# Kernel optimization log

Hardware: AMD Instinct MI355X
Metric: run time of the kernel (lower is better)

Reference implementation:

```python
import jax, jax.numpy as jnp
import numpy as np

H, W = 480, 640
NUM_CLASSES = 3
SKIP = 5            # skip_pixels: stride between voting pixels
GRID = 8            # stride of Hough accumulator bins
LABEL_THRESHOLD = 5
INLIER_THRESHOLD = 0.5
VOTING_THRESHOLD = 0.3


def setup_inputs():
    key = jax.random.key(0)
    k1, k2, k3, k4 = jax.random.split(key, 4)
    bottom_label = jax.random.randint(k1, (1, H, W), 0, NUM_CLASSES).astype(jnp.int32)
    bottom_vertex = jax.random.normal(k2, (1, NUM_CLASSES * 3, H, W), jnp.float32)
    bottom_meta_data = jax.random.normal(k3, (1, 10), jnp.float32)
    extents = jax.random.normal(k4, (NUM_CLASSES, 3), jnp.float32)
    return {"bottom_label": bottom_label, "bottom_vertex": bottom_vertex,
            "bottom_meta_data": bottom_meta_data, "extents": extents}


def _hough_voting(bottom_label, bottom_vertex, bottom_meta_data, extents):
    label = bottom_label[0]                                   # [H,W] int
    vert = bottom_vertex[0].reshape(NUM_CLASSES, 3, H, W)     # per-class (ux,uy,dist)

    # voter pixels on a SKIP-strided grid
    vy, vx = jnp.meshgrid(jnp.arange(0, H, SKIP), jnp.arange(0, W, SKIP), indexing="ij")
    vy = vy.reshape(-1)
    vx = vx.reshape(-1)                                       # [V]
    vl = label[vy, vx]                                        # voter class labels [V]
    d = vert[vl, :, vy, vx]                                   # [V,3] gather own-class prediction
    ux, uy, dist = d[:, 0], d[:, 1], d[:, 2]

    # Hough bin centers on a GRID-strided grid
    by, bx = jnp.meshgrid(jnp.arange(GRID // 2, H, GRID), jnp.arange(GRID // 2, W, GRID), indexing="ij")
    by = by.reshape(-1).astype(jnp.float32)
    bx = bx.reshape(-1).astype(jnp.float32)                   # [B]

    # per (voter, bin) agreement between predicted direction and vector to bin
    ddx = bx[None, :] - vx[:, None].astype(jnp.float32)       # [V,B]
    ddy = by[None, :] - vy[:, None].astype(jnp.float32)
    inv_n = jax.lax.rsqrt(ddx * ddx + ddy * ddy + 1e-6)
    cos = (ddx * ux[:, None] + ddy * uy[:, None]) * inv_n     # [V,B]
    w = jnp.where((cos > INLIER_THRESHOLD) & (vl[:, None] > 0), 1.0, 0.0)

    # scatter votes into per-class Hough space (class 0 = background, masked above)
    hough = jax.ops.segment_sum(w, vl, num_segments=NUM_CLASSES)                 # [C,B]
    dsum = jax.ops.segment_sum(w * dist[:, None], vl, num_segments=NUM_CLASSES)  # [C,B]
    counts = jax.ops.segment_sum(jnp.ones_like(vl, jnp.float32), vl, num_segments=NUM_CLASSES)

    # peak detection per class
    peak = jnp.argmax(hough, axis=1)                          # [C]
    votes = jnp.take_along_axis(hough, peak[:, None], axis=1)[:, 0]
    depth = jnp.take_along_axis(dsum, peak[:, None], axis=1)[:, 0] / jnp.maximum(votes, 1.0)
    cx = bx[peak]
    cy = by[peak]
    score = votes / jnp.maximum(counts, 1.0)
    valid = (counts > LABEL_THRESHOLD) & (score > VOTING_THRESHOLD)

    # project object extents through camera intrinsics at estimated depth -> box size
    fx = bottom_meta_data[0, 0]
    fy = bottom_meta_data[0, 4]
    diag = jnp.sqrt(jnp.sum(extents * extents, axis=1))       # [C]
    safe_z = jnp.maximum(jnp.abs(depth), 1e-3)
    bw = jnp.abs(diag * fx) / safe_z
    bh = jnp.abs(diag * fy) / safe_z

    cls = jnp.arange(NUM_CLASSES, dtype=jnp.float32)
    rois = jnp.stack([cls, cx - bw / 2, cy - bh / 2, cx + bw / 2, cy + bh / 2,
                      score * valid.astype(jnp.float32)], axis=1)  # [C,6]
    return rois, hough


def reference(bottom_label, bottom_vertex, bottom_meta_data, extents):
    return _hough_voting(bottom_label, bottom_vertex, bottom_meta_data, extents)
```

## Files before the change

kernel.cpp:

```cpp
#include <hip/hip_runtime.h>

#define HH 480
#define WW 640
#define NC 3
#define NVX 128
#define NVY 96
#define NV (NVX * NVY)
#define NBX 80
#define NBY 60
#define NB (NBX * NBY)
#define NPB 48
#define BINBLOCKS ((NB + 255) / 256)

__global__ void precompute_pts(const int* __restrict__ label,
                               const float* __restrict__ vert,
                               float4* __restrict__ ptsA,
                               float4* __restrict__ ptsB,
                               int* __restrict__ cnt,
                               float* __restrict__ blockCounts,
                               float* __restrict__ hough,
                               float* __restrict__ dsum) {
    __shared__ int swtot[4], sn2[4];
    const int tid = threadIdx.x;
    const int i = blockIdx.x * 256 + tid;
    const int iy = i >> 7;
    const int ix = i & (NVX - 1);
    const int pix = (5 * iy) * WW + 5 * ix;
    const int vl = label[pix];
    const float* base = vert + (size_t)(vl * 3) * HH * WW + pix;
    const float ux = base[0];
    const float uy = base[(size_t)HH * WW];
    const float dist = base[(size_t)2 * HH * WW];

    const bool pos = (vl > 0);
    const int lane = tid & 63, w = tid >> 6;
    unsigned long long mp = __ballot(pos);
    unsigned long long m2 = __ballot(vl == 2);
    int rank = __popcll(mp & ((1ull << lane) - 1ull));
    if (lane == 0) { swtot[w] = __popcll(mp); sn2[w] = __popcll(m2); }
    __syncthreads();
    int off = 0;
    for (int k = 0; k < w; ++k) off += swtot[k];
    if (pos) {
        int p = blockIdx.x * 256 + off + rank;
        ptsA[p] = make_float4((float)(5 * ix), (float)(5 * iy), ux, uy);
        float c2 = (vl == 2) ? 1.0f : 0.0f;
        ptsB[p] = make_float4((vl == 1) ? dist : 0.0f,
                              (vl == 2) ? dist : 0.0f,
                              (vl == 1) ? 1.0f : 0.0f, c2);
    }
    if (tid == 0) {
        int tot = swtot[0] + swtot[1] + swtot[2] + swtot[3];
        int n2 = sn2[0] + sn2[1] + sn2[2] + sn2[3];
        cnt[blockIdx.x] = tot;
        blockCounts[blockIdx.x * NC + 0] = (float)(256 - tot);
        blockCounts[blockIdx.x * NC + 1] = (float)(tot - n2);
        blockCounts[blockIdx.x * NC + 2] = (float)n2;
    }
    for (int k = i; k < NC * NB; k += NV) hough[k] = 0.0f;
    if (i < 2 * NB) dsum[i] = 0.0f;
}

__global__ void vote(const float4* __restrict__ ptsA,
                     const float4* __restrict__ ptsB,
                     const int* __restrict__ cnt,
                     float* __restrict__ hough,
                     float* __restrict__ dsum) {
    __shared__ float4 shA[256];
    __shared__ float4 shB[256];
    const int tid = threadIdx.x;
    const int p0 = blockIdx.y * 256;
    shA[tid] = ptsA[p0 + tid];
    shB[tid] = ptsB[p0 + tid];
    const int n = cnt[blockIdx.y];

    const int b = blockIdx.x * 256 + tid;
    const float bxf = (float)(4 + 8 * (b % NBX));
    const float byf = (float)(4 + 8 * (b / NBX));
    float h1 = 0.f, h2 = 0.f, d1 = 0.f, d2 = 0.f;
    __syncthreads();

#pragma unroll 4
    for (int j = 0; j < n; ++j) {
        float4 a = shA[j];
        float4 q = shB[j];
        float ddx = bxf - a.x;
        float ddy = byf - a.y;
        float nx  = __builtin_fmaf(ddx, ddx, __builtin_fmaf(ddy, ddy, 1e-6f));
        float dot = __builtin_fmaf(ddx, a.z, ddy * a.w);
        float s   = __builtin_fmaf(dot, dot, -0.25f * nx);
        bool v = (dot > 0.0f) & (s > 0.0f);
        if (__builtin_expect((dot > 0.0f) && (fabsf(s) < nx * 2e-5f), 0)) {
            float nxe  = __fadd_rn(__fadd_rn(__fmul_rn(ddx, ddx),
                                             __fmul_rn(ddy, ddy)), 1e-6f);
            float inve = __fdiv_rn(1.0f, __fsqrt_rn(nxe));
            float dote = __fadd_rn(__fmul_rn(ddx, a.z), __fmul_rn(ddy, a.w));
            v = __fmul_rn(dote, inve) > 0.5f;
        }
        float m = v ? 1.0f : 0.0f;
        d1 = __builtin_fmaf(m, q.x, d1);
        d2 = __builtin_fmaf(m, q.y, d2);
        h1 = __builtin_fmaf(m, q.z, h1);
        h2 = __builtin_fmaf(m, q.w, h2);
    }
    if (b < NB) {
        atomicAdd(&hough[NB + b], h1);
        atomicAdd(&hough[2 * NB + b], h2);
        atomicAdd(&dsum[b], d1);
        atomicAdd(&dsum[NB + b], d2);
    }
}

__global__ void finalize(const float* __restrict__ hough,
                         const float* __restrict__ dsum,
                         const float* __restrict__ blockCounts,
                         const float* __restrict__ meta,
                         const float* __restrict__ extents,
                         float* __restrict__ rois) {
    __shared__ unsigned long long skey[256];
    __shared__ float scnt[256];
    const int tid = threadIdx.x;
    const int c = blockIdx.x;

    float cntv = 0.0f;
    for (int i = tid; i < NPB; i += 256) cntv += blockCounts[i * NC + c];
    scnt[tid] = cntv;

    unsigned long long best = 0ull;
    for (int i = tid; i < NB; i += 256) {
        float v = hough[c * NB + i];
        unsigned long long key =
            ((unsigned long long)__float_as_uint(v) << 32) |
            (unsigned long long)(unsigned)(NB - 1 - i);
        if (key > best) best = key;
    }
    skey[tid] = best;
    __syncthreads();
    for (int s = 128; s > 0; s >>= 1) {
        if (tid < s) {
            if (skey[tid + s] > skey[tid]) skey[tid] = skey[tid + s];
            scnt[tid] += scnt[tid + s];
        }
        __syncthreads();
    }
    if (tid == 0) {
        float votes = __uint_as_float((unsigned)(skey[0] >> 32));
        int peak = NB - 1 - (int)(skey[0] & 0xffffffffull);
        float ds = (c == 0) ? 0.0f : dsum[(c - 1) * NB + peak];
        float depth = __fdiv_rn(ds, fmaxf(votes, 1.0f));
        float cx = (float)(4 + 8 * (peak % NBX));
        float cy = (float)(4 + 8 * (peak / NBX));
        float cntf = scnt[0];
        float score = __fdiv_rn(votes, fmaxf(cntf, 1.0f));
        int valid = (cntf > 5.0f) && (score > 0.3f);
        float fx = meta[0], fy = meta[4];
        float e0 = extents[c * 3 + 0];
        float e1 = extents[c * 3 + 1];
        float e2 = extents[c * 3 + 2];
        float diag = __fsqrt_rn(__fadd_rn(
            __fadd_rn(__fmul_rn(e0, e0), __fmul_rn(e1, e1)), __fmul_rn(e2, e2)));
        float sz = fmaxf(fabsf(depth), 0.001f);
        float bw = __fdiv_rn(fabsf(__fmul_rn(diag, fx)), sz);
        float bh = __fdiv_rn(fabsf(__fmul_rn(diag, fy)), sz);
        rois[c * 6 + 0] = (float)c;
        rois[c * 6 + 1] = cx - bw * 0.5f;
        rois[c * 6 + 2] = cy - bh * 0.5f;
        rois[c * 6 + 3] = cx + bw * 0.5f;
        rois[c * 6 + 4] = cy + bh * 0.5f;
        rois[c * 6 + 5] = valid ? score : 0.0f;
    }
}

extern "C" void kernel_launch(void* const* d_in, const int* in_sizes, int n_in,
                              void* d_out, int out_size, void* d_ws, size_t ws_size,
                              hipStream_t stream) {
    const int* label = (const int*)d_in[0];
    const float* vert = (const float*)d_in[1];
    const float* meta = (const float*)d_in[2];
    const float* extents = (const float*)d_in[3];
    float* out = (float*)d_out;

    char* ws = (char*)d_ws;
    float4* ptsA = (float4*)ws;
    float4* ptsB = (float4*)(ws + (size_t)NV * 16);
    float* dsum = (float*)(ws + (size_t)2 * NV * 16);
    float* blockCounts = (float*)(ws + (size_t)2 * NV * 16 + 2 * NB * 4);
    int* cnt = (int*)(ws + (size_t)2 * NV * 16 + 2 * NB * 4 + NPB * NC * 4);

    float* hough = out + NC * 6;

    precompute_pts<<<NPB, 256, 0, stream>>>(label, vert, ptsA, ptsB,
                                            cnt, blockCounts, hough, dsum);
    vote<<<dim3(BINBLOCKS, NPB), 256, 0, stream>>>(ptsA, ptsB, cnt, hough, dsum);
    finalize<<<NC, 256, 0, stream>>>(hough, dsum, blockCounts, meta, extents, out);
}
```

Baseline: 101.3 us.

## Fuse finalize into vote via last-block counter and halve voter bucket size

Voter buckets shrink from 256 to 128 pixels, doubling the number of vote blocks to improve load balance across CUs. The separate finalize kernel is removed. Its peak detection and ROI computation now run in the last vote block to finish, detected with an atomic done counter and thread fences, which saves a launch. In exchange, per-bin atomic traffic doubles, every vote block reserves extra shared memory, and the finalize work runs serially in one block.

```diff
diff --git a/kernel.cpp b/kernel.cpp
--- a/kernel.cpp
+++ b/kernel.cpp
@@ -9,8 +9,10 @@
 #define NBX 80
 #define NBY 60
 #define NB (NBX * NBY)
-#define NPB 48
+#define NBK 96
+#define BKT 128
 #define BINBLOCKS ((NB + 255) / 256)
+#define VOTEBLOCKS (BINBLOCKS * NBK)
 
 __global__ void precompute_pts(const int* __restrict__ label,
                                const float* __restrict__ vert,
@@ -19,10 +21,11 @@
                                int* __restrict__ cnt,
                                float* __restrict__ blockCounts,
                                float* __restrict__ hough,
-                               float* __restrict__ dsum) {
-    __shared__ int swtot[4], sn2[4];
+                               float* __restrict__ dsum,
+                               unsigned int* __restrict__ done) {
+    __shared__ int swtot[2], sn2[2];
     const int tid = threadIdx.x;
-    const int i = blockIdx.x * 256 + tid;
+    const int i = blockIdx.x * BKT + tid;
     const int iy = i >> 7;
     const int ix = i & (NVX - 1);
     const int pix = (5 * iy) * WW + 5 * ix;
@@ -39,39 +42,47 @@
     int rank = __popcll(mp & ((1ull << lane) - 1ull));
     if (lane == 0) { swtot[w] = __popcll(mp); sn2[w] = __popcll(m2); }
     __syncthreads();
-    int off = 0;
-    for (int k = 0; k < w; ++k) off += swtot[k];
     if (pos) {
-        int p = blockIdx.x * 256 + off + rank;
+        int p = blockIdx.x * BKT + (w ? swtot[0] : 0) + rank;
         ptsA[p] = make_float4((float)(5 * ix), (float)(5 * iy), ux, uy);
-        float c2 = (vl == 2) ? 1.0f : 0.0f;
         ptsB[p] = make_float4((vl == 1) ? dist : 0.0f,
                               (vl == 2) ? dist : 0.0f,
-                              (vl == 1) ? 1.0f : 0.0f, c2);
+                              (vl == 1) ? 1.0f : 0.0f,
+                              (vl == 2) ? 1.0f : 0.0f);
     }
     if (tid == 0) {
-        int tot = swtot[0] + swtot[1] + swtot[2] + swtot[3];
-        int n2 = sn2[0] + sn2[1] + sn2[2] + sn2[3];
+        int tot = swtot[0] + swtot[1];
+        int n2 = sn2[0] + sn2[1];
         cnt[blockIdx.x] = tot;
-        blockCounts[blockIdx.x * NC + 0] = (float)(256 - tot);
+        blockCounts[blockIdx.x * NC + 0] = (float)(BKT - tot);
         blockCounts[blockIdx.x * NC + 1] = (float)(tot - n2);
         blockCounts[blockIdx.x * NC + 2] = (float)n2;
     }
     for (int k = i; k < NC * NB; k += NV) hough[k] = 0.0f;
     if (i < 2 * NB) dsum[i] = 0.0f;
+    if (i == 0) *done = 0u;
 }
 
 __global__ void vote(const float4* __restrict__ ptsA,
                      const float4* __restrict__ ptsB,
                      const int* __restrict__ cnt,
+                     const float* __restrict__ blockCounts,
+                     const float* __restrict__ meta,
+                     const float* __restrict__ extents,
                      float* __restrict__ hough,
-                     float* __restrict__ dsum) {
-    __shared__ float4 shA[256];
-    __shared__ float4 shB[256];
+                     float* __restrict__ dsum,
+                     float* __restrict__ rois,
+                     unsigned int* __restrict__ done) {
+    __shared__ float4 shA[BKT];
+    __shared__ float4 shB[BKT];
+    __shared__ unsigned long long skey[256];
+    __shared__ float scnt[256];
+    __shared__ int slast;
+
     const int tid = threadIdx.x;
-    const int p0 = blockIdx.y * 256;
-    shA[tid] = ptsA[p0 + tid];
-    shB[tid] = ptsB[p0 + tid];
+    const int p0 = blockIdx.y * BKT;
+    if (tid < BKT) shA[tid] = ptsA[p0 + tid];
+    else           shB[tid - BKT] = ptsB[p0 + tid - BKT];
     const int n = cnt[blockIdx.y];
 
     const int b = blockIdx.x * 256 + tid;
@@ -109,65 +120,70 @@
         atomicAdd(&dsum[b], d1);
         atomicAdd(&dsum[NB + b], d2);
     }
-}
-
-__global__ void finalize(const float* __restrict__ hough,
-                         const float* __restrict__ dsum,
-                         const float* __restrict__ blockCounts,
-                         const float* __restrict__ meta,
-                         const float* __restrict__ extents,
-                         float* __restrict__ rois) {
-    __shared__ unsigned long long skey[256];
-    __shared__ float scnt[256];
-    const int tid = threadIdx.x;
-    const int c = blockIdx.x;
-
-    float cntv = 0.0f;
-    for (int i = tid; i < NPB; i += 256) cntv += blockCounts[i * NC + c];
-    scnt[tid] = cntv;
-
-    unsigned long long best = 0ull;
-    for (int i = tid; i < NB; i += 256) {
-        float v = hough[c * NB + i];
-        unsigned long long key =
-            ((unsigned long long)__float_as_uint(v) << 32) |
-            (unsigned long long)(unsigned)(NB - 1 - i);
-        if (key > best) best = key;
-    }
-    skey[tid] = best;
-    __syncthreads();
-    for (int s = 128; s > 0; s >>= 1) {
-        if (tid < s) {
-            if (skey[tid + s] > skey[tid]) skey[tid] = skey[tid + s];
-            scnt[tid] += scnt[tid + s];
-        }
+
+    __syncthreads();
+    if (tid == 0) {
+        __threadfence();
+        unsigned int old = atomicAdd(done, 1u);
+        slast = (old == VOTEBLOCKS - 1u) ? 1 : 0;
+    }
+    __syncthreads();
+    if (!slast) return;
+    __threadfence();
+
+    for (int c = 0; c < NC; ++c) {
+        float cv = 0.0f;
+        if (tid < NBK) cv = blockCounts[tid * NC + c];
+        unsigned long long best = 0ull;
+        for (int i = tid; i < NB; i += 256) {
+            float v = __hip_atomic_load(&hough[c * NB + i], __ATOMIC_RELAXED,
+                                        __HIP_MEMORY_SCOPE_AGENT);
+            unsigned long long key =
+                ((unsigned long long)__float_as_uint(v) << 32) |
+                (unsigned long long)(unsigned)(NB - 1 - i);
+            if (key > best) best = key;
+        }
+        skey[tid] = best;
+        scnt[tid] = cv;
         __syncthreads();
-    }
-    if (tid == 0) {
-        float votes = __uint_as_float((unsigned)(skey[0] >> 32));
-        int peak = NB - 1 - (int)(skey[0] & 0xffffffffull);
-        float ds = (c == 0) ? 0.0f : dsum[(c - 1) * NB + peak];
-        float depth = __fdiv_rn(ds, fmaxf(votes, 1.0f));
-        float cx = (float)(4 + 8 * (peak % NBX));
-        float cy = (float)(4 + 8 * (peak / NBX));
-        float cntf = scnt[0];
-        float score = __fdiv_rn(votes, fmaxf(cntf, 1.0f));
-        int valid = (cntf > 5.0f) && (score > 0.3f);
-        float fx = meta[0], fy = meta[4];
-        float e0 = extents[c * 3 + 0];
-        float e1 = extents[c * 3 + 1];
-        float e2 = extents[c * 3 + 2];
-        float diag = __fsqrt_rn(__fadd_rn(
-            __fadd_rn(__fmul_rn(e0, e0), __fmul_rn(e1, e1)), __fmul_rn(e2, e2)));
-        float sz = fmaxf(fabsf(depth), 0.001f);
-        float bw = __fdiv_rn(fabsf(__fmul_rn(diag, fx)), sz);
-        float bh = __fdiv_rn(fabsf(__fmul_rn(diag, fy)), sz);
-        rois[c * 6 + 0] = (float)c;
-        rois[c * 6 + 1] = cx - bw * 0.5f;
-        rois[c * 6 + 2] = cy - bh * 0.5f;
-        rois[c * 6 + 3] = cx + bw * 0.5f;
-        rois[c * 6 + 4] = cy + bh * 0.5f;
-        rois[c * 6 + 5] = valid ? score : 0.0f;
+        for (int s = 128; s > 0; s >>= 1) {
+            if (tid < s) {
+                if (skey[tid + s] > skey[tid]) skey[tid] = skey[tid + s];
+                scnt[tid] += scnt[tid + s];
+            }
+            __syncthreads();
+        }
+        if (tid == 0) {
+            float votes = __uint_as_float((unsigned)(skey[0] >> 32));
+            int peak = NB - 1 - (int)(skey[0] & 0xffffffffull);
+            float ds = (c == 0) ? 0.0f
+                     : __hip_atomic_load(&dsum[(c - 1) * NB + peak],
+                                         __ATOMIC_RELAXED,
+                                         __HIP_MEMORY_SCOPE_AGENT);
+            float depth = __fdiv_rn(ds, fmaxf(votes, 1.0f));
+            float cx = (float)(4 + 8 * (peak % NBX));
+            float cy = (float)(4 + 8 * (peak / NBX));
+            float cntf = scnt[0];
+            float score = __fdiv_rn(votes, fmaxf(cntf, 1.0f));
+            int valid = (cntf > 5.0f) && (score > 0.3f);
+            float fx = meta[0], fy = meta[4];
+            float e0 = extents[c * 3 + 0];
+            float e1 = extents[c * 3 + 1];
+            float e2 = extents[c * 3 + 2];
+            float diag = __fsqrt_rn(__fadd_rn(
+                __fadd_rn(__fmul_rn(e0, e0), __fmul_rn(e1, e1)),
+                __fmul_rn(e2, e2)));
+            float sz = fmaxf(fabsf(depth), 0.001f);
+            float bw = __fdiv_rn(fabsf(__fmul_rn(diag, fx)), sz);
+            float bh = __fdiv_rn(fabsf(__fmul_rn(diag, fy)), sz);
+            rois[c * 6 + 0] = (float)c;
+            rois[c * 6 + 1] = cx - bw * 0.5f;
+            rois[c * 6 + 2] = cy - bh * 0.5f;
+            rois[c * 6 + 3] = cx + bw * 0.5f;
+            rois[c * 6 + 4] = cy + bh * 0.5f;
+            rois[c * 6 + 5] = valid ? score : 0.0f;
+        }
+        __syncthreads();
     }
 }
 
@@ -185,12 +201,15 @@
     float4* ptsB = (float4*)(ws + (size_t)NV * 16);
     float* dsum = (float*)(ws + (size_t)2 * NV * 16);
     float* blockCounts = (float*)(ws + (size_t)2 * NV * 16 + 2 * NB * 4);
-    int* cnt = (int*)(ws + (size_t)2 * NV * 16 + 2 * NB * 4 + NPB * NC * 4);
+    int* cnt = (int*)(ws + (size_t)2 * NV * 16 + 2 * NB * 4 + NBK * NC * 4);
+    unsigned int* done = (unsigned int*)(ws + (size_t)2 * NV * 16 + 2 * NB * 4
+                                         + NBK * NC * 4 + NBK * 4);
 
     float* hough = out + NC * 6;
 
-    precompute_pts<<<NPB, 256, 0, stream>>>(label, vert, ptsA, ptsB,
-                                            cnt, blockCounts, hough, dsum);
-    vote<<<dim3(BINBLOCKS, NPB), 256, 0, stream>>>(ptsA, ptsB, cnt, hough, dsum);
-    finalize<<<NC, 256, 0, stream>>>(hough, dsum, blockCounts, meta, extents, out);
+    precompute_pts<<<NBK, BKT, 0, stream>>>(label, vert, ptsA, ptsB,
+                                            cnt, blockCounts, hough, dsum, done);
+    vote<<<dim3(BINBLOCKS, NBK), 256, 0, stream>>>(ptsA, ptsB, cnt, blockCounts,
+                                                   meta, extents, hough, dsum,
+                                                   out, done);
 }
```

Result: slower. 126.1 us (+24.5%).

## Compute two Hough bins per thread and branch on a wave-uniform voter class

Applied to the files above, without the earlier changes.

Each vote thread now handles two horizontally adjacent bins. The y-dependent terms and the shared-memory point loads are reused across both bins, and the grid shrinks to 10 x-blocks. The per-voter payload shrinks from four floats to a float2 holding depth and class id. The class is read with readfirstlane so the accumulation takes a uniform branch instead of four FMAs with mask products. In exchange there are fewer blocks in flight and more registers per thread, which may lower occupancy.

```diff
diff --git a/kernel.cpp b/kernel.cpp
--- a/kernel.cpp
+++ b/kernel.cpp
@@ -10,12 +10,12 @@
 #define NBY 60
 #define NB (NBX * NBY)
 #define NPB 48
-#define BINBLOCKS ((NB + 255) / 256)
+#define XBLK 10
 
 __global__ void precompute_pts(const int* __restrict__ label,
                                const float* __restrict__ vert,
                                float4* __restrict__ ptsA,
-                               float4* __restrict__ ptsB,
+                               float2* __restrict__ ptsB,
                                int* __restrict__ cnt,
                                float* __restrict__ blockCounts,
                                float* __restrict__ hough,
@@ -44,10 +44,8 @@
     if (pos) {
         int p = blockIdx.x * 256 + off + rank;
         ptsA[p] = make_float4((float)(5 * ix), (float)(5 * iy), ux, uy);
-        float c2 = (vl == 2) ? 1.0f : 0.0f;
-        ptsB[p] = make_float4((vl == 1) ? dist : 0.0f,
-                              (vl == 2) ? dist : 0.0f,
-                              (vl == 1) ? 1.0f : 0.0f, c2);
+        float2 pb; pb.x = dist; pb.y = __int_as_float(vl);
+        ptsB[p] = pb;
     }
     if (tid == 0) {
         int tot = swtot[0] + swtot[1] + swtot[2] + swtot[3];
@@ -62,52 +60,84 @@
 }
 
 __global__ void vote(const float4* __restrict__ ptsA,
-                     const float4* __restrict__ ptsB,
+                     const float2* __restrict__ ptsB,
                      const int* __restrict__ cnt,
                      float* __restrict__ hough,
                      float* __restrict__ dsum) {
     __shared__ float4 shA[256];
-    __shared__ float4 shB[256];
+    __shared__ float2 shB[256];
     const int tid = threadIdx.x;
     const int p0 = blockIdx.y * 256;
     shA[tid] = ptsA[p0 + tid];
     shB[tid] = ptsB[p0 + tid];
     const int n = cnt[blockIdx.y];
 
-    const int b = blockIdx.x * 256 + tid;
-    const float bxf = (float)(4 + 8 * (b % NBX));
-    const float byf = (float)(4 + 8 * (b / NBX));
-    float h1 = 0.f, h2 = 0.f, d1 = 0.f, d2 = 0.f;
+    const int b0 = 2 * (blockIdx.x * 256 + tid);
+    const float bx0 = (float)(4 + 8 * (b0 % NBX));
+    const float bx1 = bx0 + 8.0f;
+    const float byf = (float)(4 + 8 * (b0 / NBX));
+    float h10 = 0.f, h20 = 0.f, d10 = 0.f, d20 = 0.f;
+    float h11 = 0.f, h21 = 0.f, d11 = 0.f, d21 = 0.f;
     __syncthreads();
 
 #pragma unroll 4
     for (int j = 0; j < n; ++j) {
         float4 a = shA[j];
-        float4 q = shB[j];
-        float ddx = bxf - a.x;
+        float2 q = shB[j];
+        const int cls = __builtin_amdgcn_readfirstlane(__float_as_int(q.y));
+        const float z = q.x;
         float ddy = byf - a.y;
-        float nx  = __builtin_fmaf(ddx, ddx, __builtin_fmaf(ddy, ddy, 1e-6f));
-        float dot = __builtin_fmaf(ddx, a.z, ddy * a.w);
-        float s   = __builtin_fmaf(dot, dot, -0.25f * nx);
-        bool v = (dot > 0.0f) & (s > 0.0f);
-        if (__builtin_expect((dot > 0.0f) && (fabsf(s) < nx * 2e-5f), 0)) {
-            float nxe  = __fadd_rn(__fadd_rn(__fmul_rn(ddx, ddx),
-                                             __fmul_rn(ddy, ddy)), 1e-6f);
-            float inve = __fdiv_rn(1.0f, __fsqrt_rn(nxe));
-            float dote = __fadd_rn(__fmul_rn(ddx, a.z), __fmul_rn(ddy, a.w));
-            v = __fmul_rn(dote, inve) > 0.5f;
+        float dyt = __builtin_fmaf(ddy, ddy, 1e-6f);
+        float dyu = ddy * a.w;
+
+        float ddx0 = bx0 - a.x;
+        float nx0  = __builtin_fmaf(ddx0, ddx0, dyt);
+        float dot0 = __builtin_fmaf(ddx0, a.z, dyu);
+        float s0   = __builtin_fmaf(dot0, dot0, -0.25f * nx0);
+        bool v0 = (dot0 > 0.f) & (s0 > 0.f);
+
+        float ddx1 = bx1 - a.x;
+        float nx1  = __builtin_fmaf(ddx1, ddx1, dyt);
+        float dot1 = __builtin_fmaf(ddx1, a.z, dyu);
+        float s1   = __builtin_fmaf(dot1, dot1, -0.25f * nx1);
+        bool v1 = (dot1 > 0.f) & (s1 > 0.f);
+
+        if (__builtin_expect(((dot0 > 0.f) && (fabsf(s0) < nx0 * 2e-5f)) ||
+                             ((dot1 > 0.f) && (fabsf(s1) < nx1 * 2e-5f)), 0)) {
+            {
+                float nxe  = __fadd_rn(__fadd_rn(__fmul_rn(ddx0, ddx0),
+                                                 __fmul_rn(ddy, ddy)), 1e-6f);
+                float inve = __fdiv_rn(1.0f, __fsqrt_rn(nxe));
+                float dote = __fadd_rn(__fmul_rn(ddx0, a.z), __fmul_rn(ddy, a.w));
+                v0 = __fmul_rn(dote, inve) > 0.5f;
+            }
+            {
+                float nxe  = __fadd_rn(__fadd_rn(__fmul_rn(ddx1, ddx1),
+                                                 __fmul_rn(ddy, ddy)), 1e-6f);
+                float inve = __fdiv_rn(1.0f, __fsqrt_rn(nxe));
+                float dote = __fadd_rn(__fmul_rn(ddx1, a.z), __fmul_rn(ddy, a.w));
+                v1 = __fmul_rn(dote, inve) > 0.5f;
+            }
         }
-        float m = v ? 1.0f : 0.0f;
-        d1 = __builtin_fmaf(m, q.x, d1);
-        d2 = __builtin_fmaf(m, q.y, d2);
-        h1 = __builtin_fmaf(m, q.z, h1);
-        h2 = __builtin_fmaf(m, q.w, h2);
-    }
-    if (b < NB) {
-        atomicAdd(&hough[NB + b], h1);
-        atomicAdd(&hough[2 * NB + b], h2);
-        atomicAdd(&dsum[b], d1);
-        atomicAdd(&dsum[NB + b], d2);
+        float m0 = v0 ? 1.0f : 0.0f;
+        float m1 = v1 ? 1.0f : 0.0f;
+        if (cls == 1) {
+            h10 += m0; d10 = __builtin_fmaf(m0, z, d10);
+            h11 += m1; d11 = __builtin_fmaf(m1, z, d11);
+        } else {
+            h20 += m0; d20 = __builtin_fmaf(m0, z, d20);
+            h21 += m1; d21 = __builtin_fmaf(m1, z, d21);
+        }
+    }
+    if (b0 < NB) {
+        atomicAdd(&hough[NB + b0], h10);
+        atomicAdd(&hough[2 * NB + b0], h20);
+        atomicAdd(&dsum[b0], d10);
+        atomicAdd(&dsum[NB + b0], d20);
+        atomicAdd(&hough[NB + b0 + 1], h11);
+        atomicAdd(&hough[2 * NB + b0 + 1], h21);
+        atomicAdd(&dsum[b0 + 1], d11);
+        atomicAdd(&dsum[NB + b0 + 1], d21);
     }
 }
 
@@ -182,15 +212,15 @@
 
     char* ws = (char*)d_ws;
     float4* ptsA = (float4*)ws;
-    float4* ptsB = (float4*)(ws + (size_t)NV * 16);
-    float* dsum = (float*)(ws + (size_t)2 * NV * 16);
-    float* blockCounts = (float*)(ws + (size_t)2 * NV * 16 + 2 * NB * 4);
-    int* cnt = (int*)(ws + (size_t)2 * NV * 16 + 2 * NB * 4 + NPB * NC * 4);
+    float2* ptsB = (float2*)(ws + (size_t)NV * 16);
+    float* dsum = (float*)(ws + (size_t)NV * 24);
+    float* blockCounts = (float*)(ws + (size_t)NV * 24 + 2 * NB * 4);
+    int* cnt = (int*)(ws + (size_t)NV * 24 + 2 * NB * 4 + NPB * NC * 4);
 
     float* hough = out + NC * 6;
 
     precompute_pts<<<NPB, 256, 0, stream>>>(label, vert, ptsA, ptsB,
                                             cnt, blockCounts, hough, dsum);
-    vote<<<dim3(BINBLOCKS, NPB), 256, 0, stream>>>(ptsA, ptsB, cnt, hough, dsum);
+    vote<<<dim3(XBLK, NPB), 256, 0, stream>>>(ptsA, ptsB, cnt, hough, dsum);
     finalize<<<NC, 256, 0, stream>>>(hough, dsum, blockCounts, meta, extents, out);
 }
```

After: 123.9 us. 22.4% more time.

## Split voting by class into 64-point buckets, two bins per thread, deterministic reduction

Applied to the files above, without the earlier changes.

Voters are compacted into 64-wide buckets sorted by class, so the vote loop runs class-1 and class-2 points separately and drops the per-point class-weight multiplies. Each thread now evaluates two adjacent bins, sharing the dy terms. The rare exact-precision fallback moves out of the hot loop into a flagged second pass. Atomics are replaced by per-bucket partial planes that a new reduce kernel sums. This adds an extra kernel launch and roughly 15 MB of partial-buffer traffic in exchange for less ALU work per (voter, bin) pair and more grid parallelism.

```diff
diff --git a/kernel.cpp b/kernel.cpp
--- a/kernel.cpp
+++ b/kernel.cpp
@@ -9,20 +9,22 @@
 #define NBX 80
 #define NBY 60
 #define NB (NBX * NBY)
-#define NPB 48
-#define BINBLOCKS ((NB + 255) / 256)
+#define NBKT 192
+#define BKT 64
+#define PCB (NBKT / 4)
+#define XBLK 10
+#define RBLK 300
 
 __global__ void precompute_pts(const int* __restrict__ label,
                                const float* __restrict__ vert,
                                float4* __restrict__ ptsA,
-                               float4* __restrict__ ptsB,
-                               int* __restrict__ cnt,
-                               float* __restrict__ blockCounts,
-                               float* __restrict__ hough,
-                               float* __restrict__ dsum) {
-    __shared__ int swtot[4], sn2[4];
+                               float* __restrict__ ptsZ,
+                               int* __restrict__ cnts,
+                               float* __restrict__ blockCounts) {
     const int tid = threadIdx.x;
     const int i = blockIdx.x * 256 + tid;
+    const int lane = tid & 63;
+    const int bucket = i >> 6;
     const int iy = i >> 7;
     const int ix = i & (NVX - 1);
     const int pix = (5 * iy) * WW + 5 * ix;
@@ -32,82 +34,160 @@
     const float uy = base[(size_t)HH * WW];
     const float dist = base[(size_t)2 * HH * WW];
 
-    const bool pos = (vl > 0);
-    const int lane = tid & 63, w = tid >> 6;
-    unsigned long long mp = __ballot(pos);
+    unsigned long long m1 = __ballot(vl == 1);
     unsigned long long m2 = __ballot(vl == 2);
-    int rank = __popcll(mp & ((1ull << lane) - 1ull));
-    if (lane == 0) { swtot[w] = __popcll(mp); sn2[w] = __popcll(m2); }
+    const int n1 = __popcll(m1);
+    const int n2 = __popcll(m2);
+    const unsigned long long below = (1ull << lane) - 1ull;
+    int pos = -1;
+    if (vl == 1) pos = bucket * BKT + __popcll(m1 & below);
+    else if (vl == 2) pos = bucket * BKT + n1 + __popcll(m2 & below);
+    if (pos >= 0) {
+        ptsA[pos] = make_float4((float)(5 * ix), (float)(5 * iy),
+                                __fmul_rn(2.0f, ux), __fmul_rn(2.0f, uy));
+        ptsZ[pos] = dist;
+    }
+    if (lane == 0) {
+        cnts[bucket] = n1 | ((n1 + n2) << 16);
+        blockCounts[bucket * NC + 0] = (float)(BKT - n1 - n2);
+        blockCounts[bucket * NC + 1] = (float)n1;
+        blockCounts[bucket * NC + 2] = (float)n2;
+    }
+}
+
+__global__ void vote(const float4* __restrict__ ptsA,
+                     const float* __restrict__ ptsZ,
+                     const int* __restrict__ cnts,
+                     float* __restrict__ partial) {
+    __shared__ float4 shA[BKT];
+    __shared__ float shZ[BKT];
+    const int tid = threadIdx.x;
+    const int p0 = blockIdx.y * BKT;
+    if (tid < BKT) { shA[tid] = ptsA[p0 + tid]; shZ[tid] = ptsZ[p0 + tid]; }
+    const int packed = cnts[blockIdx.y];
+    const int n1 = packed & 0xffff;
+    const int nt = packed >> 16;
+
+    const int gi = blockIdx.x * 256 + tid;
+    const int b0 = 2 * gi;
+    const float bx0 = (float)(4 + 8 * (b0 % NBX));
+    const float bx1 = bx0 + 8.0f;
+    const float byf = (float)(4 + 8 * (b0 / NBX));
+    float h1a = 0.f, h1b = 0.f, d1a = 0.f, d1b = 0.f;
+    float h2a = 0.f, h2b = 0.f, d2a = 0.f, d2b = 0.f;
+    float flagacc = -1.0f;
     __syncthreads();
-    int off = 0;
-    for (int k = 0; k < w; ++k) off += swtot[k];
-    if (pos) {
-        int p = blockIdx.x * 256 + off + rank;
-        ptsA[p] = make_float4((float)(5 * ix), (float)(5 * iy), ux, uy);
-        float c2 = (vl == 2) ? 1.0f : 0.0f;
-        ptsB[p] = make_float4((vl == 1) ? dist : 0.0f,
-                              (vl == 2) ? dist : 0.0f,
-                              (vl == 1) ? 1.0f : 0.0f, c2);
-    }
-    if (tid == 0) {
-        int tot = swtot[0] + swtot[1] + swtot[2] + swtot[3];
-        int n2 = sn2[0] + sn2[1] + sn2[2] + sn2[3];
-        cnt[blockIdx.x] = tot;
-        blockCounts[blockIdx.x * NC + 0] = (float)(256 - tot);
-        blockCounts[blockIdx.x * NC + 1] = (float)(tot - n2);
-        blockCounts[blockIdx.x * NC + 2] = (float)n2;
-    }
-    for (int k = i; k < NC * NB; k += NV) hough[k] = 0.0f;
-    if (i < 2 * NB) dsum[i] = 0.0f;
-}
-
-__global__ void vote(const float4* __restrict__ ptsA,
-                     const float4* __restrict__ ptsB,
-                     const int* __restrict__ cnt,
-                     float* __restrict__ hough,
-                     float* __restrict__ dsum) {
-    __shared__ float4 shA[256];
-    __shared__ float4 shB[256];
-    const int tid = threadIdx.x;
-    const int p0 = blockIdx.y * 256;
-    shA[tid] = ptsA[p0 + tid];
-    shB[tid] = ptsB[p0 + tid];
-    const int n = cnt[blockIdx.y];
-
-    const int b = blockIdx.x * 256 + tid;
-    const float bxf = (float)(4 + 8 * (b % NBX));
-    const float byf = (float)(4 + 8 * (b / NBX));
-    float h1 = 0.f, h2 = 0.f, d1 = 0.f, d2 = 0.f;
+
+#pragma unroll 2
+    for (int j = 0; j < n1; ++j) {
+        float4 a = shA[j];
+        float z = shZ[j];
+        float ddy = __fsub_rn(byf, a.y);
+        float dyt = __builtin_fmaf(ddy, ddy, 1e-6f);
+        float dyu = __fmul_rn(ddy, a.w);
+        float ddx0 = __fsub_rn(bx0, a.x);
+        float ddx1 = __fsub_rn(bx1, a.x);
+        float nx0 = __builtin_fmaf(ddx0, ddx0, dyt);
+        float nx1 = __builtin_fmaf(ddx1, ddx1, dyt);
+        float dt0 = __builtin_fmaf(ddx0, a.z, dyu);
+        float dt1 = __builtin_fmaf(ddx1, a.z, dyu);
+        float s0 = __builtin_fmaf(dt0, dt0, -nx0);
+        float s1 = __builtin_fmaf(dt1, dt1, -nx1);
+        flagacc = fmaxf(flagacc, __builtin_fmaf(nx0, 4e-6f, -fabsf(s0)));
+        flagacc = fmaxf(flagacc, __builtin_fmaf(nx1, 4e-6f, -fabsf(s1)));
+        float m0 = (fminf(dt0, s0) > 0.0f) ? 1.0f : 0.0f;
+        float m1_ = (fminf(dt1, s1) > 0.0f) ? 1.0f : 0.0f;
+        h1a += m0; d1a = __builtin_fmaf(m0, z, d1a);
+        h1b += m1_; d1b = __builtin_fmaf(m1_, z, d1b);
+    }
+#pragma unroll 2
+    for (int j = n1; j < nt; ++j) {
+        float4 a = shA[j];
+        float z = shZ[j];
+        float ddy = __fsub_rn(byf, a.y);
+        float dyt = __builtin_fmaf(ddy, ddy, 1e-6f);
+        float dyu = __fmul_rn(ddy, a.w);
+        float ddx0 = __fsub_rn(bx0, a.x);
+        float ddx1 = __fsub_rn(bx1, a.x);
+        float nx0 = __builtin_fmaf(ddx0, ddx0, dyt);
+        float nx1 = __builtin_fmaf(ddx1, ddx1, dyt);
+        float dt0 = __builtin_fmaf(ddx0, a.z, dyu);
+        float dt1 = __builtin_fmaf(ddx1, a.z, dyu);
+        float s0 = __builtin_fmaf(dt0, dt0, -nx0);
+        float s1 = __builtin_fmaf(dt1, dt1, -nx1);
+        flagacc = fmaxf(flagacc, __builtin_fmaf(nx0, 4e-6f, -fabsf(s0)));
+        flagacc = fmaxf(flagacc, __builtin_fmaf(nx1, 4e-6f, -fabsf(s1)));
+        float m0 = (fminf(dt0, s0) > 0.0f) ? 1.0f : 0.0f;
+        float m1_ = (fminf(dt1, s1) > 0.0f) ? 1.0f : 0.0f;
+        h2a += m0; d2a = __builtin_fmaf(m0, z, d2a);
+        h2b += m1_; d2b = __builtin_fmaf(m1_, z, d2b);
+    }
+
+    if (gi >= NB / 2) flagacc = -1.0f;
+    if (flagacc > 0.0f) {
+        for (int j = 0; j < nt; ++j) {
+            float4 a = shA[j];
+            float z = shZ[j];
+            float ddy = __fsub_rn(byf, a.y);
+            float dyt = __builtin_fmaf(ddy, ddy, 1e-6f);
+            float dyu = __fmul_rn(ddy, a.w);
+#pragma unroll
+            for (int k = 0; k < 2; ++k) {
+                float bx = k ? bx1 : bx0;
+                float ddx = __fsub_rn(bx, a.x);
+                float nx = __builtin_fmaf(ddx, ddx, dyt);
+                float dt = __builtin_fmaf(ddx, a.z, dyu);
+                float s  = __builtin_fmaf(dt, dt, -nx);
+                float mf = (fminf(dt, s) > 0.0f) ? 1.0f : 0.0f;
+                float uxe = __fmul_rn(0.5f, a.z), uye = __fmul_rn(0.5f, a.w);
+                float nxe  = __fadd_rn(__fadd_rn(__fmul_rn(ddx, ddx),
+                                                 __fmul_rn(ddy, ddy)), 1e-6f);
+                float inve = __fdiv_rn(1.0f, __fsqrt_rn(nxe));
+                float dote = __fadd_rn(__fmul_rn(ddx, uxe), __fmul_rn(ddy, uye));
+                float me   = (__fmul_rn(dote, inve) > 0.5f) ? 1.0f : 0.0f;
+                float dm   = me - mf;
+                if (j < n1) {
+                    if (k == 0) { h1a += dm; d1a = __builtin_fmaf(dm, z, d1a); }
+                    else        { h1b += dm; d1b = __builtin_fmaf(dm, z, d1b); }
+                } else {
+                    if (k == 0) { h2a += dm; d2a = __builtin_fmaf(dm, z, d2a); }
+                    else        { h2b += dm; d2b = __builtin_fmaf(dm, z, d2b); }
+                }
+            }
+        }
+    }
+
+    if (gi < NB / 2) {
+        float* base = partial + (size_t)blockIdx.y * 4 * NB;
+        *(float2*)&base[0 * NB + b0] = make_float2(h1a, h1b);
+        *(float2*)&base[1 * NB + b0] = make_float2(h2a, h2b);
+        *(float2*)&base[2 * NB + b0] = make_float2(d1a, d1b);
+        *(float2*)&base[3 * NB + b0] = make_float2(d2a, d2b);
+    }
+}
+
+__global__ void reduce(const float* __restrict__ partial,
+                       float* __restrict__ hough,
+                       float* __restrict__ dsum) {
+    __shared__ float acc[4][64];
+    const int tid = threadIdx.x;
+    const int sub = tid >> 6;
+    const int idx = blockIdx.x * 64 + (tid & 63);
+    const float* p = partial + idx;
+    float s = 0.0f;
+#pragma unroll 8
+    for (int y = sub * 48; y < sub * 48 + 48; ++y) s += p[(size_t)y * 4 * NB];
+    acc[sub][tid & 63] = s;
     __syncthreads();
-
-#pragma unroll 4
-    for (int j = 0; j < n; ++j) {
-        float4 a = shA[j];
-        float4 q = shB[j];
-        float ddx = bxf - a.x;
-        float ddy = byf - a.y;
-        float nx  = __builtin_fmaf(ddx, ddx, __builtin_fmaf(ddy, ddy, 1e-6f));
-        float dot = __builtin_fmaf(ddx, a.z, ddy * a.w);
-        float s   = __builtin_fmaf(dot, dot, -0.25f * nx);
-        bool v = (dot > 0.0f) & (s > 0.0f);
-        if (__builtin_expect((dot > 0.0f) && (fabsf(s) < nx * 2e-5f), 0)) {
-            float nxe  = __fadd_rn(__fadd_rn(__fmul_rn(ddx, ddx),
-                                             __fmul_rn(ddy, ddy)), 1e-6f);
-            float inve = __fdiv_rn(1.0f, __fsqrt_rn(nxe));
-            float dote = __fadd_rn(__fmul_rn(ddx, a.z), __fmul_rn(ddy, a.w));
-            v = __fmul_rn(dote, inve) > 0.5f;
-        }
-        float m = v ? 1.0f : 0.0f;
-        d1 = __builtin_fmaf(m, q.x, d1);
-        d2 = __builtin_fmaf(m, q.y, d2);
-        h1 = __builtin_fmaf(m, q.z, h1);
-        h2 = __builtin_fmaf(m, q.w, h2);
-    }
-    if (b < NB) {
-        atomicAdd(&hough[NB + b], h1);
-        atomicAdd(&hough[2 * NB + b], h2);
-        atomicAdd(&dsum[b], d1);
-        atomicAdd(&dsum[NB + b], d2);
+    if (sub == 0) {
+        const int l = tid & 63;
+        float t = ((acc[0][l] + acc[1][l]) + acc[2][l]) + acc[3][l];
+        const int plane = idx / NB;
+        const int b = idx % NB;
+        if (plane == 0) { hough[b] = 0.0f; hough[NB + b] = t; }
+        else if (plane == 1) hough[2 * NB + b] = t;
+        else if (plane == 2) dsum[b] = t;
+        else                 dsum[NB + b] = t;
     }
 }
 
@@ -123,7 +203,7 @@
     const int c = blockIdx.x;
 
     float cntv = 0.0f;
-    for (int i = tid; i < NPB; i += 256) cntv += blockCounts[i * NC + c];
+    for (int i = tid; i < NBKT; i += 256) cntv += blockCounts[i * NC + c];
     scnt[tid] = cntv;
 
     unsigned long long best = 0ull;
@@ -181,16 +261,19 @@
     float* out = (float*)d_out;
 
     char* ws = (char*)d_ws;
-    float4* ptsA = (float4*)ws;
-    float4* ptsB = (float4*)(ws + (size_t)NV * 16);
-    float* dsum = (float*)(ws + (size_t)2 * NV * 16);
-    float* blockCounts = (float*)(ws + (size_t)2 * NV * 16 + 2 * NB * 4);
-    int* cnt = (int*)(ws + (size_t)2 * NV * 16 + 2 * NB * 4 + NPB * NC * 4);
+    size_t off = 0;
+    float4* ptsA = (float4*)(ws + off); off += (size_t)NV * 16;
+    float* ptsZ = (float*)(ws + off); off += (size_t)NV * 4;
+    float* partial = (float*)(ws + off); off += (size_t)NBKT * 4 * NB * 4;
+    float* dsum = (float*)(ws + off); off += (size_t)2 * NB * 4;
+    float* blockCounts = (float*)(ws + off); off += (size_t)NBKT * NC * 4;
+    int* cnts = (int*)(ws + off);
 
     float* hough = out + NC * 6;
 
-    precompute_pts<<<NPB, 256, 0, stream>>>(label, vert, ptsA, ptsB,
-                                            cnt, blockCounts, hough, dsum);
-    vote<<<dim3(BINBLOCKS, NPB), 256, 0, stream>>>(ptsA, ptsB, cnt, hough, dsum);
+    precompute_pts<<<PCB, 256, 0, stream>>>(label, vert, ptsA, ptsZ,
+                                            cnts, blockCounts);
+    vote<<<dim3(XBLK, NBKT), 256, 0, stream>>>(ptsA, ptsZ, cnts, partial);
+    reduce<<<RBLK, 256, 0, stream>>>(partial, hough, dsum);
     finalize<<<NC, 256, 0, stream>>>(hough, dsum, blockCounts, meta, extents, out);
 }
```

After: 106.1 us. 1.05x slower.
